# Optimization experiments

Hardware: AMD Instinct MI355X
Metric: run time of the kernel (lower is better)

## Reference

```python
import jax, jax.numpy as jnp
import numpy as np

HIDDEN = 1024
HEADS = 16
HEAD_DIM = HIDDEN // HEADS


def setup_inputs() -> dict:
    key = jax.random.key(0)
    k1, k2, k3, k4 = jax.random.split(key, 4)
    x = jax.random.normal(k1, (4, 2048, HIDDEN), dtype=jnp.float32)
    # qkv: Linear(hidden, 3*hidden, bias=False) -> weight [3*hidden, hidden]
    w_qkv = jax.random.normal(k2, (3 * HIDDEN, HIDDEN), dtype=jnp.float32) * (HIDDEN ** -0.5)
    # out_proj: Linear(hidden, hidden) with bias
    w_out = jax.random.normal(k3, (HIDDEN, HIDDEN), dtype=jnp.float32) * (HIDDEN ** -0.5)
    b_out = jax.random.normal(k4, (HIDDEN,), dtype=jnp.float32) * 0.01
    return {"x": x, "w_qkv": w_qkv, "w_out": w_out, "b_out": b_out}


def reference(x, w_qkv, w_out, b_out):
    B, N, _ = x.shape
    scale = HEAD_DIM ** -0.5
    qkv = jnp.einsum('bnc,dc->bnd', x, w_qkv)            # [B,N,3*hidden]
    qkv = qkv.reshape(B, N, 3, HEADS, HEAD_DIM)
    qkv = jnp.transpose(qkv, (2, 0, 3, 1, 4))            # [3,B,H,N,hd]
    q, k, v = qkv[0], qkv[1], qkv[2]
    att = jnp.einsum('bhxd,bhyd->bhxy', q, k) * scale    # [B,H,N,N]
    att = jax.nn.softmax(att, axis=-1)
    out = jnp.einsum('bhxy,bhyd->bhxd', att, v)          # [B,H,N,hd]
    out = jnp.transpose(out, (0, 2, 1, 3)).reshape(B, N, HIDDEN)
    out = jnp.einsum('bnc,dc->bnd', out, w_out) + b_out
    return out
```

## Files before the change

kernel.cpp:

```cpp
#include <hip/hip_runtime.h>

typedef unsigned short u16;
typedef short short8 __attribute__((ext_vector_type(8)));
typedef float f32x4 __attribute__((ext_vector_type(4)));
typedef float f32x16 __attribute__((ext_vector_type(16)));
typedef unsigned short u16x4 __attribute__((ext_vector_type(4)));
typedef unsigned int u32x4 __attribute__((ext_vector_type(4)));

#define MFMA16(a, b, c) __builtin_amdgcn_mfma_f32_16x16x32_bf16((a), (b), (c), 0, 0, 0)
#define MFMA32(a, b, c) __builtin_amdgcn_mfma_f32_32x32x16_bf16((a), (b), (c), 0, 0, 0)

#if __has_builtin(__builtin_amdgcn_exp2f)
#define EXP2F(x) __builtin_amdgcn_exp2f(x)
#else
#define EXP2F(x) exp2f(x)
#endif

__device__ __forceinline__ u16 f2bf(float f) {
    unsigned u = __builtin_bit_cast(unsigned, f);
    u += 0x7FFFu + ((u >> 16) & 1u);
    return (u16)(u >> 16);
}

__device__ __forceinline__ void async16(void* lds, const void* g) {
    __builtin_amdgcn_global_load_lds(
        (const __attribute__((address_space(1))) void*)g,
        (__attribute__((address_space(3))) void*)lds, 16, 0, 0);
}

__device__ __forceinline__ unsigned cvtpk(float lo, float hi) {
    unsigned r;
    asm("v_cvt_pk_bf16_f32 %0, %1, %2" : "=v"(r) : "v"(lo), "v"(hi));
    return r;
}
__device__ __forceinline__ void plswap(unsigned& a, unsigned& b) {
    asm("v_permlane32_swap_b32 %0, %1" : "+v"(a), "+v"(b));
}

__device__ __forceinline__ void packP(const f32x16& s, short8& f0, short8& f1) {
    u32x4 u0, u1;
    {
        unsigned a = cvtpk(s[0], s[1]), b = cvtpk(s[4], s[5]);
        plswap(a, b);
        unsigned c = cvtpk(s[2], s[3]), d = cvtpk(s[6], s[7]);
        plswap(c, d);
        u0[0] = a; u0[1] = c; u0[2] = b; u0[3] = d;
    }
    {
        unsigned a = cvtpk(s[8], s[9]), b = cvtpk(s[12], s[13]);
        plswap(a, b);
        unsigned c = cvtpk(s[10], s[11]), d = cvtpk(s[14], s[15]);
        plswap(c, d);
        u1[0] = a; u1[1] = c; u1[2] = b; u1[3] = d;
    }
    f0 = __builtin_bit_cast(short8, u0);
    f1 = __builtin_bit_cast(short8, u1);
}

__global__ __launch_bounds__(256) void cast3(const float* __restrict__ x,
                                             const float* __restrict__ wqkv,
                                             const float* __restrict__ wout,
                                             u16* __restrict__ dst) {
    const int blk = blockIdx.x;
    const float* src;
    int idx;
    float sc = 1.0f;
    u16* out;
    if (blk < 8192) {
        src = x; out = dst; idx = (blk * 256 + threadIdx.x) * 4;
    } else if (blk < 11264) {
        src = wqkv; out = dst + (size_t)8192 * 1024;
        idx = ((blk - 8192) * 256 + threadIdx.x) * 4;
        if (idx < 1024 * 1024) sc = 0.18033688011112042f;
    } else {
        src = wout; out = dst + (size_t)11264 * 1024;
        idx = ((blk - 11264) * 256 + threadIdx.x) * 4;
    }
    float4 v = *(const float4*)(src + idx);
    u16x4 r;
    r[0] = f2bf(v.x * sc); r[1] = f2bf(v.y * sc);
    r[2] = f2bf(v.z * sc); r[3] = f2bf(v.w * sc);
    *(u16x4*)(out + idx) = r;
}

__global__ __launch_bounds__(512, 2) void gemm256(const u16* __restrict__ A,
                                                  const u16* __restrict__ B,
                                                  u16* __restrict__ qk) {
    __shared__ u16 lds[2][2][16384];
    const int tid = threadIdx.x;
    const int l = tid & 63;
    const int w = tid >> 6;
    const int g = l >> 4, lo = l & 15;
    const int wrow = w >> 2, wcol = w & 3;
    const int xcd = blockIdx.x & 7, j = blockIdx.x >> 3;
    const int tm = xcd * 4 + (j & 3), tn = j >> 2;
    const int rowBase = tm << 8, colBase = tn << 8;

    const int srow = tid >> 3;
    const int scol = (((tid * 16) ^ (((tid >> 3) & 7) << 4)) & 127) >> 1;
    const u16* pa = A + (size_t)(rowBase + srow) * 1024 + scol;
    const u16* pb = B + (size_t)(colBase + srow) * 1024 + scol;
    const int ldsOff = tid * 16;

    int abase[2], bbase[2];
#pragma unroll
    for (int k = 0; k < 2; ++k) {
        abase[k] = (((wrow * 128 + lo) * 128 + k * 64 + g * 16) ^ ((lo & 7) << 4));
        bbase[k] = (((wcol * 64 + lo) * 128 + k * 64 + g * 16) ^ ((lo & 7) << 4));
    }

    f32x4 acc[8][4] = {};

#define STAGE256(buf, kt)                                                                   \
    {                                                                                       \
        const u16* sa = pa + (kt) * 64;                                                     \
        const u16* sb = pb + (kt) * 64;                                                     \
        _Pragma("unroll")                                                                   \
        for (int i = 0; i < 4; ++i) {                                                       \
            async16((char*)lds[buf][0] + ldsOff + i * 8192, sa + (size_t)i * 64 * 1024);    \
            async16((char*)lds[buf][1] + ldsOff + i * 8192, sb + (size_t)i * 64 * 1024);    \
        }                                                                                   \
    }

    STAGE256(0, 0);
    __syncthreads();

    for (int kt = 0; kt < 16; ++kt) {
        const int cur = kt & 1;
        if (kt < 15) STAGE256(cur ^ 1, kt + 1);
        const char* la = (const char*)lds[cur][0];
        const char* lb = (const char*)lds[cur][1];

        short8 bf[4][2], af[4][2];
#pragma unroll
        for (int n = 0; n < 4; ++n)
#pragma unroll
            for (int k = 0; k < 2; ++k)
                bf[n][k] = *(const short8*)(lb + bbase[k] + n * 2048);
#pragma unroll
        for (int m = 0; m < 4; ++m)
#pragma unroll
            for (int k = 0; k < 2; ++k)
                af[m][k] = *(const short8*)(la + abase[k] + m * 2048);
        __builtin_amdgcn_s_setprio(1);
#pragma unroll
        for (int m = 0; m < 4; ++m)
#pragma unroll
            for (int n = 0; n < 4; ++n) {
                acc[m][n] = MFMA16(af[m][0], bf[n][0], acc[m][n]);
                acc[m][n] = MFMA16(af[m][1], bf[n][1], acc[m][n]);
            }
        __builtin_amdgcn_s_setprio(0);
#pragma unroll
        for (int m = 0; m < 4; ++m)
#pragma unroll
            for (int k = 0; k < 2; ++k)
                af[m][k] = *(const short8*)(la + abase[k] + (m + 4) * 2048);
        __builtin_amdgcn_s_setprio(1);
#pragma unroll
        for (int m = 0; m < 4; ++m)
#pragma unroll
            for (int n = 0; n < 4; ++n) {
                acc[m + 4][n] = MFMA16(af[m][0], bf[n][0], acc[m + 4][n]);
                acc[m + 4][n] = MFMA16(af[m][1], bf[n][1], acc[m + 4][n]);
            }
        __builtin_amdgcn_s_setprio(0);
        __syncthreads();
    }
#undef STAGE256

#pragma unroll
    for (int n = 0; n < 4; ++n) {
        const int c = colBase + wcol * 64 + n * 16 + lo;
#pragma unroll
        for (int m = 0; m < 8; ++m) {
            const int r0 = rowBase + wrow * 128 + m * 16 + g * 4;
#pragma unroll
            for (int i = 0; i < 4; ++i)
                qk[(size_t)(r0 + i) * 2048 + c] = f2bf(acc[m][n][i]);
        }
    }
}

__global__ __launch_bounds__(256, 2) void gemmV(const u16* __restrict__ A,
                                                const u16* __restrict__ Bv,
                                                u16* __restrict__ vt) {
    __shared__ u16 As[128 * 32];
    __shared__ u16 Bs[128 * 32];
    const int tid = threadIdx.x;
    const int w = tid >> 6, l = tid & 63;
    const int g = l >> 4, lo = l & 15;
    const int xcd = blockIdx.x & 7, j = blockIdx.x >> 3;
    const int tm = xcd * 8 + (j & 7), tn = j >> 3;
    const int rowBase = tm << 7, colBase = tn << 7;
    const int wrow = w >> 1, wcol = w & 1;

    f32x4 acc[4][4] = {};

    const int srow = l >> 2;
    const int scol = (l & 3) * 8;
    for (int kt = 0; kt < 32; ++kt) {
        const int kbase = kt * 32 + scol;
#pragma unroll
        for (int it = 0; it < 2; ++it) {
            const int seg = it * 4 + w;
            const int r = seg * 16 + srow;
            async16(&As[seg * 512], &A[(size_t)(rowBase + r) * 1024 + kbase]);
            async16(&Bs[seg * 512], &Bv[(size_t)(colBase + r) * 1024 + kbase]);
        }
        __syncthreads();
        short8 af[4], bf[4];
#pragma unroll
        for (int mi = 0; mi < 4; ++mi)
            af[mi] = *(const short8*)&As[(wrow * 64 + mi * 16 + lo) * 32 + g * 8];
#pragma unroll
        for (int ni = 0; ni < 4; ++ni)
            bf[ni] = *(const short8*)&Bs[(wcol * 64 + ni * 16 + lo) * 32 + g * 8];
#pragma unroll
        for (int mi = 0; mi < 4; ++mi)
#pragma unroll
            for (int ni = 0; ni < 4; ++ni)
                acc[mi][ni] = MFMA16(af[mi], bf[ni], acc[mi][ni]);
        __syncthreads();
    }

    const int b = rowBase >> 11;
#pragma unroll
    for (int ni = 0; ni < 4; ++ni) {
        const int c = colBase + wcol * 64 + ni * 16 + lo;
        const int hh = c >> 6, d = c & 63;
        u16* vrow = vt + ((size_t)((b * 16 + hh) * 64 + d)) * 2048;
#pragma unroll
        for (int mi = 0; mi < 4; ++mi) {
            const int r0 = rowBase + wrow * 64 + mi * 16 + g * 4;
            u16x4 pk;
#pragma unroll
            for (int i = 0; i < 4; ++i) pk[i] = f2bf(acc[mi][ni][i]);
            *(u16x4*)(vrow + (r0 & 2047)) = pk;
        }
    }
}

__global__ __launch_bounds__(256, 2) void gemm_bt(const u16* __restrict__ A,
                                                  const u16* __restrict__ B,
                                                  float* __restrict__ Cf,
                                                  const float* __restrict__ bias,
                                                  int M, int N, int K) {
    __shared__ u16 As[128 * 32];
    __shared__ u16 Bs[128 * 32];
    const int tid = threadIdx.x;
    const int w = tid >> 6, l = tid & 63;
    const int g = l >> 4, lo = l & 15;
    const int mtiles = M >> 7;
    const int S = mtiles >> 3;
    const int xcd = blockIdx.x & 7, j = blockIdx.x >> 3;
    const int tm = xcd * S + (j % S), tn = j / S;
    const int rowBase = tm << 7, colBase = tn << 7;
    const int wrow = w >> 1, wcol = w & 1;

    f32x4 acc[4][4] = {};

    const int srow = l >> 2;
    const int scol = (l & 3) * 8;
    const int nk = K >> 5;
    for (int kt = 0; kt < nk; ++kt) {
        const int kbase = kt * 32 + scol;
#pragma unroll
        for (int it = 0; it < 2; ++it) {
            const int seg = it * 4 + w;
            const int r = seg * 16 + srow;
            async16(&As[seg * 512], &A[(size_t)(rowBase + r) * K + kbase]);
            async16(&Bs[seg * 512], &B[(size_t)(colBase + r) * K + kbase]);
        }
        __syncthreads();
        short8 af[4], bf[4];
#pragma unroll
        for (int mi = 0; mi < 4; ++mi)
            af[mi] = *(const short8*)&As[(wrow * 64 + mi * 16 + lo) * 32 + g * 8];
#pragma unroll
        for (int ni = 0; ni < 4; ++ni)
            bf[ni] = *(const short8*)&Bs[(wcol * 64 + ni * 16 + lo) * 32 + g * 8];
#pragma unroll
        for (int mi = 0; mi < 4; ++mi)
#pragma unroll
            for (int ni = 0; ni < 4; ++ni)
                acc[mi][ni] = MFMA16(af[mi], bf[ni], acc[mi][ni]);
        __syncthreads();
    }

#pragma unroll
    for (int ni = 0; ni < 4; ++ni) {
        const int c = colBase + wcol * 64 + ni * 16 + lo;
        const float bv = bias[c];
#pragma unroll
        for (int mi = 0; mi < 4; ++mi) {
            const int r0 = rowBase + wrow * 64 + mi * 16 + g * 4;
#pragma unroll
            for (int i = 0; i < 4; ++i)
                Cf[(size_t)(r0 + i) * N + c] = acc[mi][ni][i] + bv;
        }
    }
}

__global__ __launch_bounds__(256, 4) void attn_fwd(const u16* __restrict__ qkb,
                                                   const u16* __restrict__ vtg,
                                                   u16* __restrict__ outb) {
    __shared__ u16 Ks[2][64 * 64];
    __shared__ u16 Vs[2][64 * 64];
    const int tid = threadIdx.x;
    const int w = tid >> 6, l = tid & 63;
    const int hi = l >> 5, lq = l & 31;

    const int lin = (blockIdx.x & 7) * 128 + (blockIdx.x >> 3);
    const int bh = lin >> 4, qt = lin & 15;
    const int b = bh >> 4, h = bh & 15;
    const size_t rowQ = (size_t)b * 2048 + qt * 128 + w * 32;

    short8 qf[4];
#pragma unroll
    for (int ks = 0; ks < 4; ++ks)
        qf[ks] = *(const short8*)(qkb + (rowQ + lq) * 2048 + h * 64 + ks * 16 + hi * 8);

    int koff[4];
#pragma unroll
    for (int ks = 0; ks < 4; ++ks)
        koff[ks] = (lq * 128 + ks * 32 + hi * 16) ^ ((lq & 7) << 4);

    const int L0 = tid * 16, L1 = tid * 16 + 4096;
    const int kr0 = L0 >> 7, kc0 = ((L0 ^ ((kr0 & 7) << 4)) & 127) >> 1;
    const int kr1 = L1 >> 7, kc1 = ((L1 ^ ((kr1 & 7) << 4)) & 127) >> 1;
    const u16* ks0 = qkb + (size_t)(b * 2048 + kr0) * 2048 + 1024 + h * 64 + kc0;
    const u16* ks1 = qkb + (size_t)(b * 2048 + kr1) * 2048 + 1024 + h * 64 + kc1;
    const u16* vs0 = vtg + ((size_t)bh * 64 + kr0) * 2048 + kc0;
    const u16* vs1 = vtg + ((size_t)bh * 64 + kr1) * 2048 + kc1;
    const size_t KADV = (size_t)64 * 2048;

    f32x16 O0, O1, Ol;
#pragma unroll
    for (int i = 0; i < 16; ++i) { O0[i] = 0.f; O1[i] = 0.f; Ol[i] = 0.f; }
    const f32x16 Z = {};
    const short8 onesv = {16256, 16256, 16256, 16256, 16256, 16256, 16256, 16256};

    async16((char*)Ks[0] + L0, ks0); async16((char*)Ks[0] + L1, ks1);
    async16((char*)Vs[0] + L0, vs0); async16((char*)Vs[0] + L1, vs1);
    ks0 += KADV; ks1 += KADV; vs0 += 64; vs1 += 64;

    int cur = 0;
    for (int kt = 0; kt < 32; ++kt) {
        __syncthreads();
        if (kt < 31) {
            const int nx = cur ^ 1;
            async16((char*)Ks[nx] + L0, ks0); async16((char*)Ks[nx] + L1, ks1);
            async16((char*)Vs[nx] + L0, vs0); async16((char*)Vs[nx] + L1, vs1);
            ks0 += KADV; ks1 += KADV; vs0 += 64; vs1 += 64;
        }
        const char* kb = (const char*)Ks[cur];
        const char* vb = (const char*)Vs[cur];

#pragma unroll
        for (int t = 0; t < 2; ++t) {
            const int tb = t * 4096;
            __builtin_amdgcn_s_setprio(1);
            f32x16 s = MFMA32(*(const short8*)(kb + koff[0] + tb), qf[0], Z);
            s = MFMA32(*(const short8*)(kb + koff[1] + tb), qf[1], s);
            s = MFMA32(*(const short8*)(kb + koff[2] + tb), qf[2], s);
            s = MFMA32(*(const short8*)(kb + koff[3] + tb), qf[3], s);
            __builtin_amdgcn_s_setprio(0);

#pragma unroll
            for (int i = 0; i < 16; ++i) s[i] = EXP2F(s[i]);

            short8 p0, p1;
            packP(s, p0, p1);

            __builtin_amdgcn_s_setprio(1);
            Ol = MFMA32(p0, onesv, Ol);
            Ol = MFMA32(p1, onesv, Ol);
            O0 = MFMA32(p0, *(const short8*)(vb + koff[t * 2]), O0);
            O1 = MFMA32(p0, *(const short8*)(vb + koff[t * 2] + 4096), O1);
            O0 = MFMA32(p1, *(const short8*)(vb + koff[t * 2 + 1]), O0);
            O1 = MFMA32(p1, *(const short8*)(vb + koff[t * 2 + 1] + 4096), O1);
            __builtin_amdgcn_s_setprio(0);
        }
        cur ^= 1;
    }

#pragma unroll
    for (int r = 0; r < 16; ++r) {
        const int qrow = (r & 3) + 8 * (r >> 2) + 4 * hi;
        const float linv = 1.0f / Ol[r];
        u16* op = outb + (rowQ + qrow) * 1024 + h * 64 + lq;
        op[0] = f2bf(O0[r] * linv);
        op[32] = f2bf(O1[r] * linv);
    }
}

extern "C" void kernel_launch(void* const* d_in, const int* in_sizes, int n_in,
                              void* d_out, int out_size, void* d_ws, size_t ws_size,
                              hipStream_t stream) {
    const float* x     = (const float*)d_in[0];
    const float* w_qkv = (const float*)d_in[1];
    const float* w_out = (const float*)d_in[2];
    const float* b_out = (const float*)d_in[3];
    float* out = (float*)d_out;

    u16* xb    = (u16*)d_ws;
    u16* wqkvb = xb    + (size_t)8192 * 1024;
    u16* woutb = wqkvb + (size_t)3072 * 1024;
    u16* qkb   = woutb + (size_t)1024 * 1024;
    u16* vtg   = qkb   + (size_t)8192 * 2048;
    u16* attb  = vtg   + (size_t)64 * 64 * 2048;

    cast3<<<12288, 256, 0, stream>>>(x, w_qkv, w_out, xb);

    gemm256<<<256, 512, 0, stream>>>(xb, wqkvb, qkb);
    gemmV<<<512, 256, 0, stream>>>(xb, wqkvb + (size_t)2048 * 1024, vtg);

    attn_fwd<<<1024, 256, 0, stream>>>(qkb, vtg, attb);

    gemm_bt<<<dim3((8192 / 128) * (1024 / 128)), 256, 0, stream>>>(
        attb, woutb, out, b_out, 8192, 1024, 1024);
}
```

Measured before the change: 186.3 us.

## Process two query tiles per attention block to reuse K/V LDS fragments

The attention kernel now handles 256 query rows per block instead of 128, with each wave computing two 32-row query groups against the same K and V fragments read from LDS once. This halves the grid to 512 blocks and halves global K/V loads and LDS reads per query row. In exchange it doubles the accumulator registers, lowers the launch-bounds occupancy target to 2, and leaves fewer blocks for filling the GPU.

```diff
diff --git a/kernel.cpp b/kernel.cpp
--- a/kernel.cpp
+++ b/kernel.cpp
@@ -302,7 +302,7 @@
     }
 }
 
-__global__ __launch_bounds__(256, 4) void attn_fwd(const u16* __restrict__ qkb,
+__global__ __launch_bounds__(256, 2) void attn_fwd(const u16* __restrict__ qkb,
                                                    const u16* __restrict__ vtg,
                                                    u16* __restrict__ outb) {
     __shared__ u16 Ks[2][64 * 64];
@@ -311,15 +311,18 @@
     const int w = tid >> 6, l = tid & 63;
     const int hi = l >> 5, lq = l & 31;
 
-    const int lin = (blockIdx.x & 7) * 128 + (blockIdx.x >> 3);
-    const int bh = lin >> 4, qt = lin & 15;
+    const int lin = (blockIdx.x & 7) * 64 + (blockIdx.x >> 3);
+    const int bh = lin >> 3, qt = lin & 7;
     const int b = bh >> 4, h = bh & 15;
-    const size_t rowQ = (size_t)b * 2048 + qt * 128 + w * 32;
-
-    short8 qf[4];
-#pragma unroll
-    for (int ks = 0; ks < 4; ++ks)
-        qf[ks] = *(const short8*)(qkb + (rowQ + lq) * 2048 + h * 64 + ks * 16 + hi * 8);
+    const size_t rowQ0 = (size_t)b * 2048 + qt * 256 + w * 32;
+    const size_t rowQ1 = rowQ0 + 128;
+
+    short8 qf0[4], qf1[4];
+#pragma unroll
+    for (int ks = 0; ks < 4; ++ks) {
+        qf0[ks] = *(const short8*)(qkb + (rowQ0 + lq) * 2048 + h * 64 + ks * 16 + hi * 8);
+        qf1[ks] = *(const short8*)(qkb + (rowQ1 + lq) * 2048 + h * 64 + ks * 16 + hi * 8);
+    }
 
     int koff[4];
 #pragma unroll
@@ -335,9 +338,12 @@
     const u16* vs1 = vtg + ((size_t)bh * 64 + kr1) * 2048 + kc1;
     const size_t KADV = (size_t)64 * 2048;
 
-    f32x16 O0, O1, Ol;
-#pragma unroll
-    for (int i = 0; i < 16; ++i) { O0[i] = 0.f; O1[i] = 0.f; Ol[i] = 0.f; }
+    f32x16 O00, O01, Ol0, O10, O11, Ol1;
+#pragma unroll
+    for (int i = 0; i < 16; ++i) {
+        O00[i] = 0.f; O01[i] = 0.f; Ol0[i] = 0.f;
+        O10[i] = 0.f; O11[i] = 0.f; Ol1[i] = 0.f;
+    }
     const f32x16 Z = {};
     const short8 onesv = {16256, 16256, 16256, 16256, 16256, 16256, 16256, 16256};
 
@@ -360,27 +366,55 @@
 #pragma unroll
         for (int t = 0; t < 2; ++t) {
             const int tb = t * 4096;
-            __builtin_amdgcn_s_setprio(1);
-            f32x16 s = MFMA32(*(const short8*)(kb + koff[0] + tb), qf[0], Z);
-            s = MFMA32(*(const short8*)(kb + koff[1] + tb), qf[1], s);
-            s = MFMA32(*(const short8*)(kb + koff[2] + tb), qf[2], s);
-            s = MFMA32(*(const short8*)(kb + koff[3] + tb), qf[3], s);
-            __builtin_amdgcn_s_setprio(0);
-
-#pragma unroll
-            for (int i = 0; i < 16; ++i) s[i] = EXP2F(s[i]);
-
-            short8 p0, p1;
-            packP(s, p0, p1);
-
-            __builtin_amdgcn_s_setprio(1);
-            Ol = MFMA32(p0, onesv, Ol);
-            Ol = MFMA32(p1, onesv, Ol);
-            O0 = MFMA32(p0, *(const short8*)(vb + koff[t * 2]), O0);
-            O1 = MFMA32(p0, *(const short8*)(vb + koff[t * 2] + 4096), O1);
-            O0 = MFMA32(p1, *(const short8*)(vb + koff[t * 2 + 1]), O0);
-            O1 = MFMA32(p1, *(const short8*)(vb + koff[t * 2 + 1] + 4096), O1);
-            __builtin_amdgcn_s_setprio(0);
+            short8 kf0 = *(const short8*)(kb + koff[0] + tb);
+            short8 kf1 = *(const short8*)(kb + koff[1] + tb);
+            short8 kf2 = *(const short8*)(kb + koff[2] + tb);
+            short8 kf3 = *(const short8*)(kb + koff[3] + tb);
+            short8 vfa = *(const short8*)(vb + koff[t * 2]);
+            short8 vfb = *(const short8*)(vb + koff[t * 2] + 4096);
+            short8 vfc = *(const short8*)(vb + koff[t * 2 + 1]);
+            short8 vfd = *(const short8*)(vb + koff[t * 2 + 1] + 4096);
+
+            {
+                __builtin_amdgcn_s_setprio(1);
+                f32x16 s = MFMA32(kf0, qf0[0], Z);
+                s = MFMA32(kf1, qf0[1], s);
+                s = MFMA32(kf2, qf0[2], s);
+                s = MFMA32(kf3, qf0[3], s);
+                __builtin_amdgcn_s_setprio(0);
+#pragma unroll
+                for (int i = 0; i < 16; ++i) s[i] = EXP2F(s[i]);
+                short8 p0, p1;
+                packP(s, p0, p1);
+                __builtin_amdgcn_s_setprio(1);
+                Ol0 = MFMA32(p0, onesv, Ol0);
+                Ol0 = MFMA32(p1, onesv, Ol0);
+                O00 = MFMA32(p0, vfa, O00);
+                O01 = MFMA32(p0, vfb, O01);
+                O00 = MFMA32(p1, vfc, O00);
+                O01 = MFMA32(p1, vfd, O01);
+                __builtin_amdgcn_s_setprio(0);
+            }
+            {
+                __builtin_amdgcn_s_setprio(1);
+                f32x16 s = MFMA32(kf0, qf1[0], Z);
+                s = MFMA32(kf1, qf1[1], s);
+                s = MFMA32(kf2, qf1[2], s);
+                s = MFMA32(kf3, qf1[3], s);
+                __builtin_amdgcn_s_setprio(0);
+#pragma unroll
+                for (int i = 0; i < 16; ++i) s[i] = EXP2F(s[i]);
+                short8 p0, p1;
+                packP(s, p0, p1);
+                __builtin_amdgcn_s_setprio(1);
+                Ol1 = MFMA32(p0, onesv, Ol1);
+                Ol1 = MFMA32(p1, onesv, Ol1);
+                O10 = MFMA32(p0, vfa, O10);
+                O11 = MFMA32(p0, vfb, O11);
+                O10 = MFMA32(p1, vfc, O10);
+                O11 = MFMA32(p1, vfd, O11);
+                __builtin_amdgcn_s_setprio(0);
+            }
         }
         cur ^= 1;
     }
@@ -388,10 +422,18 @@
 #pragma unroll
     for (int r = 0; r < 16; ++r) {
         const int qrow = (r & 3) + 8 * (r >> 2) + 4 * hi;
-        const float linv = 1.0f / Ol[r];
-        u16* op = outb + (rowQ + qrow) * 1024 + h * 64 + lq;
-        op[0] = f2bf(O0[r] * linv);
-        op[32] = f2bf(O1[r] * linv);
+        {
+            const float linv = 1.0f / Ol0[r];
+            u16* op = outb + (rowQ0 + qrow) * 1024 + h * 64 + lq;
+            op[0] = f2bf(O00[r] * linv);
+            op[32] = f2bf(O01[r] * linv);
+        }
+        {
+            const float linv = 1.0f / Ol1[r];
+            u16* op = outb + (rowQ1 + qrow) * 1024 + h * 64 + lq;
+            op[0] = f2bf(O10[r] * linv);
+            op[32] = f2bf(O11[r] * linv);
+        }
     }
 }
 
@@ -416,7 +458,7 @@
     gemm256<<<256, 512, 0, stream>>>(xb, wqkvb, qkb);
     gemmV<<<512, 256, 0, stream>>>(xb, wqkvb + (size_t)2048 * 1024, vtg);
 
-    attn_fwd<<<1024, 256, 0, stream>>>(qkb, vtg, attb);
+    attn_fwd<<<512, 256, 0, stream>>>(qkb, vtg, attb);
 
     gemm_bt<<<dim3((8192 / 128) * (1024 / 128)), 256, 0, stream>>>(
         attb, woutb, out, b_out, 8192, 1024, 1024);
```

After: 180.8 us. 3.0% less time.
